# Performance work log

Hardware: AMD Instinct MI355X
Metric: run time of the kernel (lower is better)

Reference implementation:

```python
import jax, jax.numpy as jnp
import numpy as np

SIG_G = (1.0, 1.0, 1.0)  # Cl(3,0) metric signature -> 2^3 = 8 blades


def build_cayley(g):
    """Cayley table C[p, q, k] for the Clifford geometric product.
    Blades indexed by bitmasks; e_A * e_B = sign * metric * e_{A^B}."""
    n = len(g)
    nb = 1 << n
    C = np.zeros((nb, nb, nb), dtype=np.float32)
    for a in range(nb):
        for b in range(nb):
            # reordering sign: move generators of b past higher-index generators of a
            swaps = 0
            t = a >> 1
            while t:
                swaps += bin(t & b).count('1')
                t >>= 1
            s = -1.0 if (swaps & 1) else 1.0
            # metric contribution from repeated generators (e_i e_i = g_i)
            for i in range(n):
                if (a >> i) & 1 and (b >> i) & 1:
                    s *= g[i]
            C[a, b, a ^ b] = s
    return jnp.asarray(C)


def geometric_product(x, w, cayley):
    # x: [B, I, P blades], w: [O, I, Q blades] -> y: [B, O, K blades]
    return jnp.einsum('bip,oiq,pqk->bok', x, w, cayley)


def setup_inputs() -> dict:
    key = jax.random.key(0)
    kx, k1, k2, k3 = jax.random.split(key, 4)
    B, D, NB = 2048, 512, 8
    x = jax.random.normal(kx, (B, D, NB), dtype=jnp.float32)
    w1 = 0.1 * jax.random.normal(k1, (D, D, NB), dtype=jnp.float32)
    w2 = 0.1 * jax.random.normal(k2, (D, D, NB), dtype=jnp.float32)
    w3 = 0.1 * jax.random.normal(k3, (D, D, NB), dtype=jnp.float32)
    return {'x': x, 'w1': w1, 'w2': w2, 'w3': w3}


def reference(x, w1, w2, w3):
    cayley = build_cayley(SIG_G)  # [8, 8, 8], sparse Cayley table (constant)
    acts = [x]
    for w in (w1, w2, w3):
        acts.append(geometric_product(acts[-1], w, cayley))
    # original forward returns the list of activations; all share a shape here,
    # so stack to a single [L+1, B, D, NB] array
    return jnp.stack(acts, axis=0)
```

## Files before the change

### kernel.cpp

```cpp
#include <hip/hip_runtime.h>

using u16    = unsigned short;
using u32    = unsigned int;
using bf16x8 = __attribute__((ext_vector_type(8))) __bf16;
using f32x4  = __attribute__((ext_vector_type(4))) float;
using u16x4  = __attribute__((ext_vector_type(4))) u16;
using u16x8  = __attribute__((ext_vector_type(8))) u16;

__device__ __forceinline__ u16 f32_to_bf16(float f) {
    u32 u = __float_as_uint(f);
    u32 r = (u + 0x7FFFu + ((u >> 16) & 1u)) >> 16;
    return (u16)r;
}

__device__ __forceinline__ void gld_lds16(const void* g, void* l) {
    __builtin_amdgcn_global_load_lds(
        (const __attribute__((address_space(1))) u32*)g,
        (__attribute__((address_space(3))) u32*)l,
        16, 0, 0);
}

__device__ __forceinline__ float cl3_sign(int a, int b) {
    int swaps = __popc((a >> 1) & b) + __popc((a >> 2) & b);
    return (swaps & 1) ? -1.0f : 1.0f;
}

__global__ __launch_bounds__(256) void prep_kernel(
    const float* __restrict__ x, float* __restrict__ out0, u16* __restrict__ A0)
{
    const int t = blockIdx.x * 256 + threadIdx.x;
    const float4 v = reinterpret_cast<const float4*>(x)[t];
    reinterpret_cast<float4*>(out0)[t] = v;
    u16x4 b;
    b.x = f32_to_bf16(v.x);
    b.y = f32_to_bf16(v.y);
    b.z = f32_to_bf16(v.z);
    b.w = f32_to_bf16(v.w);
    reinterpret_cast<u16x4*>(A0)[t] = b;
}

__global__ __launch_bounds__(256) void expand_kernel(
    const float* __restrict__ w, u16* __restrict__ Wm)
{
    const int t = blockIdx.x * 256 + threadIdx.x;
    const int o = t >> 9;
    const int i = t & 511;
    const float* src = w + ((size_t)t << 3);
    const float4 w0 = reinterpret_cast<const float4*>(src)[0];
    const float4 w1 = reinterpret_cast<const float4*>(src)[1];
    const float wv[8] = {w0.x, w0.y, w0.z, w0.w, w1.x, w1.y, w1.z, w1.w};
    #pragma unroll
    for (int kb = 0; kb < 8; ++kb) {
        u16x8 ov;
        #pragma unroll
        for (int p = 0; p < 8; ++p) {
            const int q = p ^ kb;
            ov[p] = f32_to_bf16(cl3_sign(p, q) * wv[q]);
        }
        reinterpret_cast<u16x8*>(Wm)[((size_t)(o * 8 + kb) << 9) + i] = ov;
    }
}

constexpr int BM = 128, BN = 256, BK = 64, KDIM = 4096, NKT = KDIM / BK;
constexpr int ASZ = BM * BK;
constexpr int BSZ = BN * BK;
constexpr int BUF = ASZ + BSZ;

__global__ __launch_bounds__(512, 2) void gemm8_kernel(
    const u16* __restrict__ A,
    const u16* __restrict__ Bt,
    float*     __restrict__ C,
    u16*       __restrict__ An)
{
    __shared__ __attribute__((aligned(16))) u16 lds[3 * BUF];

    const int tid = threadIdx.x;
    const int l   = tid & 63;
    const int w   = tid >> 6;
    const int wr  = w >> 2;
    const int wc  = w & 3;
    const int l8  = l >> 3, l7 = l & 7;
    const int fr  = l & 15, fq = l >> 4;
    const int row0 = blockIdx.y * BM;
    const int col0 = blockIdx.x * BN;

    auto stageA = [&](int buf, int kt, int q) {
        const int g = q * 8 + w;
        const int r = g * 8 + l8;
        const u16* src = A + (size_t)(row0 + r) * KDIM + kt + ((l7 ^ l8) << 3);
        gld_lds16(src, &lds[buf * BUF + r * BK + l7 * 8]);
    };
    auto stageB = [&](int buf, int kt, int q) {
        const int g = q * 8 + w;
        const int r = g * 8 + l8;
        const u16* src = Bt + (size_t)(col0 + r) * KDIM + kt + ((l7 ^ l8) << 3);
        gld_lds16(src, &lds[buf * BUF + ASZ + r * BK + l7 * 8]);
    };
    auto rdA = [&](int buf, int mi, int ks) -> bf16x8 {
        const int r = wr * 64 + mi * 16 + fr;
        const int c = (ks * 4 + fq) ^ (r & 7);
        return *reinterpret_cast<const bf16x8*>(&lds[buf * BUF + r * BK + c * 8]);
    };
    auto rdB = [&](int buf, int ni, int ks) -> bf16x8 {
        const int r = wc * 64 + ni * 16 + fr;
        const int c = (ks * 4 + fq) ^ (r & 7);
        return *reinterpret_cast<const bf16x8*>(&lds[buf * BUF + ASZ + r * BK + c * 8]);
    };

    f32x4 acc[4][4];
    #pragma unroll
    for (int i = 0; i < 4; ++i)
        #pragma unroll
        for (int j = 0; j < 4; ++j)
            acc[i][j] = f32x4{0.f, 0.f, 0.f, 0.f};

    stageA(0, 0, 0); stageA(0, 0, 1);
    stageB(0, 0, 0); stageB(0, 0, 1); stageB(0, 0, 2); stageB(0, 0, 3);
    stageA(1, BK, 0); stageA(1, BK, 1);
    stageB(1, BK, 0); stageB(1, BK, 1); stageB(1, BK, 2); stageB(1, BK, 3);
    asm volatile("s_waitcnt vmcnt(6)" ::: "memory");
    __builtin_amdgcn_s_barrier();

    bf16x8 a0[2][2], a1[2][2], b0[2][2], b1[2][2];

    int cb = 0, nb = 2;
    for (int t = 0; t < NKT; ++t) {
        const int kt2 = (t + 2) * BK;
        const bool pre = (t + 2 < NKT);

        #pragma unroll
        for (int mi = 0; mi < 2; ++mi)
            #pragma unroll
            for (int ks = 0; ks < 2; ++ks) a0[mi][ks] = rdA(cb, mi, ks);
        #pragma unroll
        for (int ni = 0; ni < 2; ++ni)
            #pragma unroll
            for (int ks = 0; ks < 2; ++ks) b0[ni][ks] = rdB(cb, ni, ks);
        if (pre) { stageA(nb, kt2, 0); stageA(nb, kt2, 1); }
        __builtin_amdgcn_s_barrier();
        asm volatile("s_waitcnt lgkmcnt(0)" ::: "memory");
        __builtin_amdgcn_sched_barrier(0);
        __builtin_amdgcn_s_setprio(1);
        #pragma unroll
        for (int mi = 0; mi < 2; ++mi)
            #pragma unroll
            for (int ni = 0; ni < 2; ++ni)
                #pragma unroll
                for (int ks = 0; ks < 2; ++ks)
                    acc[mi][ni] = __builtin_amdgcn_mfma_f32_16x16x32_bf16(
                        a0[mi][ks], b0[ni][ks], acc[mi][ni], 0, 0, 0);
        __builtin_amdgcn_s_setprio(0);
        __builtin_amdgcn_s_barrier();

        #pragma unroll
        for (int ni = 0; ni < 2; ++ni)
            #pragma unroll
            for (int ks = 0; ks < 2; ++ks) b1[ni][ks] = rdB(cb, ni + 2, ks);
        if (pre) { stageB(nb, kt2, 0); stageB(nb, kt2, 1); }
        __builtin_amdgcn_s_barrier();
        asm volatile("s_waitcnt lgkmcnt(0)" ::: "memory");
        __builtin_amdgcn_sched_barrier(0);
        __builtin_amdgcn_s_setprio(1);
        #pragma unroll
        for (int mi = 0; mi < 2; ++mi)
            #pragma unroll
            for (int ni = 0; ni < 2; ++ni)
                #pragma unroll
                for (int ks = 0; ks < 2; ++ks)
                    acc[mi][ni + 2] = __builtin_amdgcn_mfma_f32_16x16x32_bf16(
                        a0[mi][ks], b1[ni][ks], acc[mi][ni + 2], 0, 0, 0);
        __builtin_amdgcn_s_setprio(0);
        __builtin_amdgcn_s_barrier();

        #pragma unroll
        for (int mi = 0; mi < 2; ++mi)
            #pragma unroll
            for (int ks = 0; ks < 2; ++ks) a1[mi][ks] = rdA(cb, mi + 2, ks);
        if (pre) { stageB(nb, kt2, 2); stageB(nb, kt2, 3); }
        __builtin_amdgcn_s_barrier();
        asm volatile("s_waitcnt lgkmcnt(0)" ::: "memory");
        __builtin_amdgcn_sched_barrier(0);
        __builtin_amdgcn_s_setprio(1);
        #pragma unroll
        for (int mi = 0; mi < 2; ++mi)
            #pragma unroll
            for (int ni = 0; ni < 2; ++ni)
                #pragma unroll
                for (int ks = 0; ks < 2; ++ks)
                    acc[mi + 2][ni + 2] = __builtin_amdgcn_mfma_f32_16x16x32_bf16(
                        a1[mi][ks], b1[ni][ks], acc[mi + 2][ni + 2], 0, 0, 0);
        __builtin_amdgcn_s_setprio(0);
        __builtin_amdgcn_s_barrier();

        #pragma unroll
        for (int ni = 0; ni < 2; ++ni)
            #pragma unroll
            for (int ks = 0; ks < 2; ++ks) b0[ni][ks] = rdB(cb, ni, ks);
        __builtin_amdgcn_s_barrier();
        asm volatile("s_waitcnt lgkmcnt(0)" ::: "memory");
        __builtin_amdgcn_sched_barrier(0);
        __builtin_amdgcn_s_setprio(1);
        #pragma unroll
        for (int mi = 0; mi < 2; ++mi)
            #pragma unroll
            for (int ni = 0; ni < 2; ++ni)
                #pragma unroll
                for (int ks = 0; ks < 2; ++ks)
                    acc[mi + 2][ni] = __builtin_amdgcn_mfma_f32_16x16x32_bf16(
                        a1[mi][ks], b0[ni][ks], acc[mi + 2][ni], 0, 0, 0);
        __builtin_amdgcn_s_setprio(0);
        if (t + 2 < NKT)      { asm volatile("s_waitcnt vmcnt(6)" ::: "memory"); }
        else if (t + 1 < NKT) { asm volatile("s_waitcnt vmcnt(0)" ::: "memory"); }
        __builtin_amdgcn_s_barrier();

        cb = (cb == 2) ? 0 : cb + 1;
        nb = (nb == 2) ? 0 : nb + 1;
    }

    #pragma unroll
    for (int mi = 0; mi < 4; ++mi) {
        #pragma unroll
        for (int v = 0; v < 4; ++v) {
            const int r = row0 + wr * 64 + mi * 16 + fq * 4 + v;
            const size_t base = ((size_t)r << 12) + col0 + wc * 64 + fr;
            #pragma unroll
            for (int ni = 0; ni < 4; ++ni)
                C[base + ni * 16] = acc[mi][ni][v];
            if (An != nullptr) {
                #pragma unroll
                for (int ni = 0; ni < 4; ++ni)
                    An[base + ni * 16] = f32_to_bf16(acc[mi][ni][v]);
            }
        }
    }
}

extern "C" void kernel_launch(void* const* d_in, const int* in_sizes, int n_in,
                              void* d_out, int out_size, void* d_ws, size_t ws_size,
                              hipStream_t stream) {
    const float* x = (const float*)d_in[0];
    const float* wts[3] = {(const float*)d_in[1], (const float*)d_in[2],
                           (const float*)d_in[3]};
    float* out = (float*)d_out;

    constexpr size_t LAYER = (size_t)2048 * 4096;

    u16* A0 = (u16*)d_ws;
    u16* A1 = A0 + LAYER;
    u16* Wm = A1 + LAYER;

    prep_kernel<<<dim3(8192), dim3(256), 0, stream>>>(x, out, A0);

    u16* Ac = A0;
    u16* Anx = A1;
    for (int L = 0; L < 3; ++L) {
        expand_kernel<<<dim3(1024), dim3(256), 0, stream>>>(wts[L], Wm);
        gemm8_kernel<<<dim3(16, 16), dim3(512), 0, stream>>>(
            Ac, Wm, out + (size_t)(L + 1) * LAYER, (L == 2) ? nullptr : Anx);
        u16* t = Ac; Ac = Anx; Anx = t;
    }
}
```

Measured before the change: 394.3 us.

## Restructure GEMM inner loop into two phases and batch weight expansion

The GEMM main loop drops from four LDS-read/MFMA phases per K-tile to two. Each phase loads two A fragments and all four B fragments, which cuts barriers per iteration while holding more B registers live. The three per-layer weight-expansion launches are merged into one launch writing three separate expanded-weight buffers, used only when the workspace is large enough. This removes two launches and the serialization between expansion and GEMM, at the cost of more workspace memory.

Result: slower. 421.9 us (+7.0%).

```diff
diff --git a/kernel.cpp b/kernel.cpp
--- a/kernel.cpp
+++ b/kernel.cpp
@@ -39,10 +39,9 @@
     reinterpret_cast<u16x4*>(A0)[t] = b;
 }
 
-__global__ __launch_bounds__(256) void expand_kernel(
-    const float* __restrict__ w, u16* __restrict__ Wm)
-{
-    const int t = blockIdx.x * 256 + threadIdx.x;
+__device__ __forceinline__ void expand_body(
+    const float* __restrict__ w, u16* __restrict__ Wm, int t)
+{
     const int o = t >> 9;
     const int i = t & 511;
     const float* src = w + ((size_t)t << 3);
@@ -61,6 +60,24 @@
     }
 }
 
+__global__ __launch_bounds__(256) void expand3_kernel(
+    const float* __restrict__ wa, const float* __restrict__ wb,
+    const float* __restrict__ wc,
+    u16* __restrict__ Wa, u16* __restrict__ Wb, u16* __restrict__ Wc)
+{
+    const int bb = blockIdx.x;
+    const int Lw = bb >> 10;
+    const float* w = (Lw == 0) ? wa : (Lw == 1) ? wb : wc;
+    u16* Wm       = (Lw == 0) ? Wa : (Lw == 1) ? Wb : Wc;
+    expand_body(w, Wm, (bb & 1023) * 256 + threadIdx.x);
+}
+
+__global__ __launch_bounds__(256) void expand_kernel(
+    const float* __restrict__ w, u16* __restrict__ Wm)
+{
+    expand_body(w, Wm, blockIdx.x * 256 + threadIdx.x);
+}
+
 constexpr int BM = 128, BN = 256, BK = 64, KDIM = 4096, NKT = KDIM / BK;
 constexpr int ASZ = BM * BK;
 constexpr int BSZ = BN * BK;
@@ -85,14 +102,12 @@
     const int col0 = blockIdx.x * BN;
 
     auto stageA = [&](int buf, int kt, int q) {
-        const int g = q * 8 + w;
-        const int r = g * 8 + l8;
+        const int r = (q * 8 + w) * 8 + l8;
         const u16* src = A + (size_t)(row0 + r) * KDIM + kt + ((l7 ^ l8) << 3);
         gld_lds16(src, &lds[buf * BUF + r * BK + l7 * 8]);
     };
     auto stageB = [&](int buf, int kt, int q) {
-        const int g = q * 8 + w;
-        const int r = g * 8 + l8;
+        const int r = (q * 8 + w) * 8 + l8;
         const u16* src = Bt + (size_t)(col0 + r) * KDIM + kt + ((l7 ^ l8) << 3);
         gld_lds16(src, &lds[buf * BUF + ASZ + r * BK + l7 * 8]);
     };
@@ -121,7 +136,7 @@
     asm volatile("s_waitcnt vmcnt(6)" ::: "memory");
     __builtin_amdgcn_s_barrier();
 
-    bf16x8 a0[2][2], a1[2][2], b0[2][2], b1[2][2];
+    bf16x8 a[2][2], b[4][2];
 
     int cb = 0, nb = 2;
     for (int t = 0; t < NKT; ++t) {
@@ -131,12 +146,12 @@
         #pragma unroll
         for (int mi = 0; mi < 2; ++mi)
             #pragma unroll
-            for (int ks = 0; ks < 2; ++ks) a0[mi][ks] = rdA(cb, mi, ks);
-        #pragma unroll
-        for (int ni = 0; ni < 2; ++ni)
-            #pragma unroll
-            for (int ks = 0; ks < 2; ++ks) b0[ni][ks] = rdB(cb, ni, ks);
-        if (pre) { stageA(nb, kt2, 0); stageA(nb, kt2, 1); }
+            for (int ks = 0; ks < 2; ++ks) a[mi][ks] = rdA(cb, mi, ks);
+        #pragma unroll
+        for (int ni = 0; ni < 4; ++ni)
+            #pragma unroll
+            for (int ks = 0; ks < 2; ++ks) b[ni][ks] = rdB(cb, ni, ks);
+        if (pre) { stageA(nb, kt2, 0); stageA(nb, kt2, 1); stageB(nb, kt2, 0); }
         __builtin_amdgcn_s_barrier();
         asm volatile("s_waitcnt lgkmcnt(0)" ::: "memory");
         __builtin_amdgcn_sched_barrier(0);
@@ -144,19 +159,19 @@
         #pragma unroll
         for (int mi = 0; mi < 2; ++mi)
             #pragma unroll
-            for (int ni = 0; ni < 2; ++ni)
+            for (int ni = 0; ni < 4; ++ni)
                 #pragma unroll
                 for (int ks = 0; ks < 2; ++ks)
                     acc[mi][ni] = __builtin_amdgcn_mfma_f32_16x16x32_bf16(
-                        a0[mi][ks], b0[ni][ks], acc[mi][ni], 0, 0, 0);
+                        a[mi][ks], b[ni][ks], acc[mi][ni], 0, 0, 0);
         __builtin_amdgcn_s_setprio(0);
         __builtin_amdgcn_s_barrier();
 
         #pragma unroll
-        for (int ni = 0; ni < 2; ++ni)
-            #pragma unroll
-            for (int ks = 0; ks < 2; ++ks) b1[ni][ks] = rdB(cb, ni + 2, ks);
-        if (pre) { stageB(nb, kt2, 0); stageB(nb, kt2, 1); }
+        for (int mi = 0; mi < 2; ++mi)
+            #pragma unroll
+            for (int ks = 0; ks < 2; ++ks) a[mi][ks] = rdA(cb, mi + 2, ks);
+        if (pre) { stageB(nb, kt2, 1); stageB(nb, kt2, 2); stageB(nb, kt2, 3); }
         __builtin_amdgcn_s_barrier();
         asm volatile("s_waitcnt lgkmcnt(0)" ::: "memory");
         __builtin_amdgcn_sched_barrier(0);
@@ -164,50 +179,11 @@
         #pragma unroll
         for (int mi = 0; mi < 2; ++mi)
             #pragma unroll
-            for (int ni = 0; ni < 2; ++ni)
-                #pragma unroll
-                for (int ks = 0; ks < 2; ++ks)
-                    acc[mi][ni + 2] = __builtin_amdgcn_mfma_f32_16x16x32_bf16(
-                        a0[mi][ks], b1[ni][ks], acc[mi][ni + 2], 0, 0, 0);
-        __builtin_amdgcn_s_setprio(0);
-        __builtin_amdgcn_s_barrier();
-
-        #pragma unroll
-        for (int mi = 0; mi < 2; ++mi)
-            #pragma unroll
-            for (int ks = 0; ks < 2; ++ks) a1[mi][ks] = rdA(cb, mi + 2, ks);
-        if (pre) { stageB(nb, kt2, 2); stageB(nb, kt2, 3); }
-        __builtin_amdgcn_s_barrier();
-        asm volatile("s_waitcnt lgkmcnt(0)" ::: "memory");
-        __builtin_amdgcn_sched_barrier(0);
-        __builtin_amdgcn_s_setprio(1);
-        #pragma unroll
-        for (int mi = 0; mi < 2; ++mi)
-            #pragma unroll
-            for (int ni = 0; ni < 2; ++ni)
-                #pragma unroll
-                for (int ks = 0; ks < 2; ++ks)
-                    acc[mi + 2][ni + 2] = __builtin_amdgcn_mfma_f32_16x16x32_bf16(
-                        a1[mi][ks], b1[ni][ks], acc[mi + 2][ni + 2], 0, 0, 0);
-        __builtin_amdgcn_s_setprio(0);
-        __builtin_amdgcn_s_barrier();
-
-        #pragma unroll
-        for (int ni = 0; ni < 2; ++ni)
-            #pragma unroll
-            for (int ks = 0; ks < 2; ++ks) b0[ni][ks] = rdB(cb, ni, ks);
-        __builtin_amdgcn_s_barrier();
-        asm volatile("s_waitcnt lgkmcnt(0)" ::: "memory");
-        __builtin_amdgcn_sched_barrier(0);
-        __builtin_amdgcn_s_setprio(1);
-        #pragma unroll
-        for (int mi = 0; mi < 2; ++mi)
-            #pragma unroll
-            for (int ni = 0; ni < 2; ++ni)
+            for (int ni = 0; ni < 4; ++ni)
                 #pragma unroll
                 for (int ks = 0; ks < 2; ++ks)
                     acc[mi + 2][ni] = __builtin_amdgcn_mfma_f32_16x16x32_bf16(
-                        a1[mi][ks], b0[ni][ks], acc[mi + 2][ni], 0, 0, 0);
+                        a[mi][ks], b[ni][ks], acc[mi + 2][ni], 0, 0, 0);
         __builtin_amdgcn_s_setprio(0);
         if (t + 2 < NKT)      { asm volatile("s_waitcnt vmcnt(6)" ::: "memory"); }
         else if (t + 1 < NKT) { asm volatile("s_waitcnt vmcnt(0)" ::: "memory"); }
@@ -244,19 +220,33 @@
     float* out = (float*)d_out;
 
     constexpr size_t LAYER = (size_t)2048 * 4096;
+    constexpr size_t WSZ   = (size_t)4096 * 4096;
 
     u16* A0 = (u16*)d_ws;
     u16* A1 = A0 + LAYER;
-    u16* Wm = A1 + LAYER;
 
     prep_kernel<<<dim3(8192), dim3(256), 0, stream>>>(x, out, A0);
 
+    const bool fused = ws_size >= (2 * LAYER + 3 * WSZ) * sizeof(u16);
     u16* Ac = A0;
     u16* Anx = A1;
-    for (int L = 0; L < 3; ++L) {
-        expand_kernel<<<dim3(1024), dim3(256), 0, stream>>>(wts[L], Wm);
-        gemm8_kernel<<<dim3(16, 16), dim3(512), 0, stream>>>(
-            Ac, Wm, out + (size_t)(L + 1) * LAYER, (L == 2) ? nullptr : Anx);
-        u16* t = Ac; Ac = Anx; Anx = t;
-    }
-}
+
+    if (fused) {
+        u16* Wm[3] = {A1 + LAYER, A1 + LAYER + WSZ, A1 + LAYER + 2 * WSZ};
+        expand3_kernel<<<dim3(3072), dim3(256), 0, stream>>>(
+            wts[0], wts[1], wts[2], Wm[0], Wm[1], Wm[2]);
+        for (int L = 0; L < 3; ++L) {
+            gemm8_kernel<<<dim3(16, 16), dim3(512), 0, stream>>>(
+                Ac, Wm[L], out + (size_t)(L + 1) * LAYER, (L == 2) ? nullptr : Anx);
+            u16* t = Ac; Ac = Anx; Anx = t;
+        }
+    } else {
+        u16* Wm = A1 + LAYER;
+        for (int L = 0; L < 3; ++L) {
+            expand_kernel<<<dim3(1024), dim3(256), 0, stream>>>(wts[L], Wm);
+            gemm8_kernel<<<dim3(16, 16), dim3(512), 0, stream>>>(
+                Ac, Wm, out + (size_t)(L + 1) * LAYER, (L == 2) ? nullptr : Anx);
+            u16* t = Ac; Ac = Anx; Anx = t;
+        }
+    }
+}
```
